# Kernel tuning notes

Measured on AMD Instinct MI355X. Metric: run time of the kernel, lower is better.

The kernel has to match this reference:

```python
import math
import jax, jax.numpy as jnp
import numpy as np

B, N, DIM_IN, DIM_OUT = 16, 2048, 512, 512
D_K, N_HEADS = 10, 2
D_HEAD = D_K // N_HEADS  # 5


def setup_inputs() -> dict:
    key = jax.random.key(0)
    ks = jax.random.split(key, 11)
    s_in = 1.0 / math.sqrt(DIM_IN)
    s_dk = 1.0 / math.sqrt(D_K)
    s_20 = 1.0 / math.sqrt(20)
    return {
        "x": jax.random.normal(ks[0], (B, N, DIM_IN), jnp.float32),
        "Wq": jax.random.normal(ks[1], (DIM_IN, D_K), jnp.float32) * s_in,
        "bq": jax.random.normal(ks[2], (D_K,), jnp.float32) * s_in,
        "Wk": jax.random.normal(ks[3], (DIM_IN, D_K), jnp.float32) * s_in,
        "bk": jax.random.normal(ks[4], (D_K,), jnp.float32) * s_in,
        "Wv": jax.random.normal(ks[5], (DIM_IN, D_K), jnp.float32) * s_in,
        "bv": jax.random.normal(ks[6], (D_K,), jnp.float32) * s_in,
        "Wm1": jax.random.normal(ks[7], (D_K, 20), jnp.float32) * s_dk,
        "bm1": jax.random.normal(ks[8], (20,), jnp.float32) * s_dk,
        "Wm2": jax.random.normal(ks[9], (20, DIM_OUT), jnp.float32) * s_20,
        "bm2": jax.random.normal(ks[10], (DIM_OUT,), jnp.float32) * s_20,
    }


def reference(x, Wq, bq, Wk, bk, Wv, bv, Wm1, bm1, Wm2, bm2):
    b, n, _ = x.shape
    # project and split heads: [B, n, d_k] -> [B, h, n, d_head]
    def heads(w, bias):
        return (x @ w + bias).reshape(b, n, N_HEADS, D_HEAD).transpose(0, 2, 1, 3)
    q, k, v = heads(Wq, bq), heads(Wk, bk), heads(Wv, bv)
    # sin-activated scores, then causal mask + softmax
    scores = jnp.sin(jnp.einsum("bhqd,bhkd->bhqk", q, k) / math.sqrt(D_HEAD))
    causal = jnp.tril(jnp.ones((n, n), bool))  # nopeak mask, k=0
    scores = jnp.where(causal, scores, jnp.float32(-1e9))
    attn = jax.nn.softmax(scores, axis=-1)
    vals = jnp.einsum("bhqk,bhkd->bhqd", attn, v)
    concat = vals.transpose(0, 2, 1, 3).reshape(b, n, D_K)
    # MLP head: leaky_relu (slope 0.01) then linear
    h1 = jax.nn.leaky_relu(concat @ Wm1 + bm1, negative_slope=0.01)
    return h1 @ Wm2 + bm2
```

## Files before the change

### kernel.cpp

```cpp
#include <hip/hip_runtime.h>
#include <math.h>

#define BB   16
#define NN   2048
#define DIN  512
#define DKK  10
#define NHD  2
#define DH   5
#define HID  20
#define DOUT 512
#define BH   32
#define KC   256
#define NKC  8
#define PC   64
#define QB   512

#define QKV_ELEMS  ((size_t)3*BH*NN*8)
#define PART_ELEMS ((size_t)NKC*BH*NN*8)

__global__ __launch_bounds__(256) void pack_w_kernel(
    const float* __restrict__ Wq, const float* __restrict__ Wk,
    const float* __restrict__ Wv, float* __restrict__ Wpack)
{
    const int idx = blockIdx.x*256 + threadIdx.x;
    const int j = idx >> 5, c = idx & 31;
    float v = 0.f;
    if (c < 10)      v = Wq[j*DKK + c];
    else if (c < 20) v = Wk[j*DKK + (c-10)];
    else if (c < 30) v = Wv[j*DKK + (c-20)];
    Wpack[idx] = v;
}

__global__ __launch_bounds__(256) void proj_kernel(
    const float* __restrict__ x, const float* __restrict__ Wpack,
    const float* __restrict__ bq, const float* __restrict__ bk,
    const float* __restrict__ bv, float* __restrict__ qkv)
{
    __shared__ float xs[PC][65];
    const int t    = threadIdx.x;
    const int lane = t & 63;
    const int grp  = __builtin_amdgcn_readfirstlane(t >> 6);
    const int tok0 = blockIdx.x*64;

    float acc[8];
    #pragma unroll
    for (int i=0;i<8;i++) acc[i]=0.f;

    for (int ch=0; ch<DIN/PC; ++ch){
        __syncthreads();
        #pragma unroll
        for (int p=0;p<4;p++){
            const int f  = t + p*256;
            const int tt = f >> 4;
            const int dd = (f & 15) * 4;
            const float4 v = *(const float4*)(x + (size_t)(tok0+tt)*DIN + ch*PC + dd);
            xs[dd+0][tt]=v.x; xs[dd+1][tt]=v.y; xs[dd+2][tt]=v.z; xs[dd+3][tt]=v.w;
        }
        __syncthreads();

        const float* wbase = Wpack + (size_t)(ch*PC)*32 + grp*8;
        for (int k=0;k<PC;k+=4){
            float w[4][8]; float xv[4];
            #pragma unroll
            for (int i=0;i<4;i++){
                xv[i] = xs[k+i][lane];
                #pragma unroll
                for (int o=0;o<8;o++) w[i][o] = wbase[(size_t)(k+i)*32+o];
            }
            #pragma unroll
            for (int i=0;i<4;i++){
                #pragma unroll
                for (int o=0;o<8;o++) acc[o] = fmaf(xv[i], w[i][o], acc[o]);
            }
        }
    }

    const float qs = 0.44721359549995793f;
    const int tok = tok0 + lane;
    const int b   = tok >> 11;
    const int n   = tok & (NN-1);
    #pragma unroll
    for (int i=0;i<8;i++){
        const int c = grp*8 + i;
        if (c >= 30) continue;
        const int mat = c / 10;
        const int d10 = c - mat*10;
        const int h   = d10 / 5;
        const int dd  = d10 - h*5;
        float v = acc[i] + ((mat==0) ? bq[d10] : (mat==1) ? bk[d10] : bv[d10]);
        if (mat==0) v *= qs;
        qkv[(size_t)mat*BH*NN*8 + (((size_t)(b*NHD+h))*NN + n)*8 + dd] = v;
    }
}

__global__ __launch_bounds__(256) void attn_kernel(
    const float* __restrict__ qkv, float* __restrict__ part)
{
    const int qt = blockIdx.x;
    const int kc = blockIdx.y;
    const int bh = blockIdx.z;
    const int k0 = kc*KC;
    const int qb0 = qt*QB;
    if (k0 >= qb0 + QB) return;

    const int w    = threadIdx.x >> 6;
    const int lane = threadIdx.x & 63;
    const int qw0  = qb0 + w*128;
    if (k0 >= qw0 + 128) return;

    const int q0 = qw0 + lane;
    const int q1 = qw0 + 64 + lane;
    const float* qr0 = qkv + ((size_t)bh*NN + q0)*8;
    const float* qr1 = qkv + ((size_t)bh*NN + q1)*8;
    const float4 qv0 = *(const float4*)qr0; const float q40 = qr0[4];
    const float4 qv1 = *(const float4*)qr1; const float q41 = qr1[4];

    const float* kb = qkv + (size_t)BH*NN*8 + (size_t)bh*NN*8;
    const float* vb = kb + (size_t)BH*NN*8;
    const int kend = min(KC, qw0 + 128 - k0);

    float d0=0,a00=0,a01=0,a02=0,a03=0,a04=0;
    float d1=0,a10=0,a11=0,a12=0,a13=0,a14=0;
    for (int kk=0; kk<kend; kk+=4){
        float4 K4[4], V4[4]; float K1[4], V1[4];
        #pragma unroll
        for (int i=0;i<4;i++){
            const float* kr = kb + (size_t)(k0+kk+i)*8;
            const float* vr = vb + (size_t)(k0+kk+i)*8;
            K4[i]=*(const float4*)kr; K1[i]=kr[4];
            V4[i]=*(const float4*)vr; V1[i]=vr[4];
        }
        #pragma unroll
        for (int i=0;i<4;i++){
            const int kg = k0+kk+i;
            float s0 = qv0.x*K4[i].x + qv0.y*K4[i].y + qv0.z*K4[i].z
                     + qv0.w*K4[i].w + q40*K1[i];
            float s1 = qv1.x*K4[i].x + qv1.y*K4[i].y + qv1.z*K4[i].z
                     + qv1.w*K4[i].w + q41*K1[i];
            float e0 = __expf(__sinf(s0));
            float e1 = __expf(__sinf(s1));
            e0 = (kg <= q0) ? e0 : 0.f;
            e1 = (kg <= q1) ? e1 : 0.f;
            d0 += e0;
            a00 = fmaf(e0, V4[i].x, a00);
            a01 = fmaf(e0, V4[i].y, a01);
            a02 = fmaf(e0, V4[i].z, a02);
            a03 = fmaf(e0, V4[i].w, a03);
            a04 = fmaf(e0, V1[i],   a04);
            d1 += e1;
            a10 = fmaf(e1, V4[i].x, a10);
            a11 = fmaf(e1, V4[i].y, a11);
            a12 = fmaf(e1, V4[i].z, a12);
            a13 = fmaf(e1, V4[i].w, a13);
            a14 = fmaf(e1, V1[i],   a14);
        }
    }
    float* pr0 = part + (((size_t)kc*BH + bh)*NN + q0)*8;
    *(float4*)pr0 = make_float4(a00,a01,a02,a03);
    pr0[4] = a04; pr0[5] = d0;
    float* pr1 = part + (((size_t)kc*BH + bh)*NN + q1)*8;
    *(float4*)pr1 = make_float4(a10,a11,a12,a13);
    pr1[4] = a14; pr1[5] = d1;
}

__global__ __launch_bounds__(256) void h1_kernel(
    const float* __restrict__ part,
    const float* __restrict__ Wm1, const float* __restrict__ bm1,
    float* __restrict__ h1buf)
{
    const int tok = blockIdx.x*256 + threadIdx.x;
    const int b   = tok >> 11;
    const int n   = tok & (NN-1);
    const int nc  = (n >> 8) + 1;

    float vals[DKK];
    #pragma unroll
    for (int h=0;h<NHD;h++){
        const int bh = b*NHD + h;
        float s0=0,s1=0,s2=0,s3=0,s4=0,sd=0;
        for (int c=0;c<nc;c++){
            const float* pr = part + (((size_t)c*BH + bh)*NN + n)*8;
            const float4 p0 = *(const float4*)pr;
            const float4 p1 = *(const float4*)(pr+4);
            s0+=p0.x; s1+=p0.y; s2+=p0.z; s3+=p0.w; s4+=p1.x; sd+=p1.y;
        }
        const float inv = 1.0f / sd;
        vals[h*DH+0]=s0*inv; vals[h*DH+1]=s1*inv; vals[h*DH+2]=s2*inv;
        vals[h*DH+3]=s3*inv; vals[h*DH+4]=s4*inv;
    }

    float h1[HID];
    #pragma unroll
    for (int jo=0;jo<HID;jo++){
        float t = bm1[jo];
        #pragma unroll
        for (int d=0;d<DKK;d++) t = fmaf(vals[d], Wm1[d*HID+jo], t);
        h1[jo] = (t > 0.f) ? t : 0.01f*t;
    }
    float* hr = h1buf + (size_t)tok*HID;
    #pragma unroll
    for (int j5=0;j5<5;j5++)
        *(float4*)(hr + j5*4) = make_float4(h1[j5*4+0],h1[j5*4+1],h1[j5*4+2],h1[j5*4+3]);
}

__global__ __launch_bounds__(256) void out_kernel(
    const float* __restrict__ h1buf,
    const float* __restrict__ Wm2, const float* __restrict__ bm2,
    float* __restrict__ out)
{
    const int wave = threadIdx.x >> 6;
    const int lane = threadIdx.x & 63;
    const int unit = blockIdx.x*4 + wave;
    const int hc   = unit & 1;
    const int tg   = unit >> 1;
    const int o0   = hc*256 + lane*4;

    float4 w2[HID];
    #pragma unroll
    for (int j=0;j<HID;j++) w2[j] = *(const float4*)(Wm2 + j*DOUT + o0);
    const float4 b2 = *(const float4*)(bm2 + o0);

    for (int ti=0; ti<8; ++ti){
        const int tok = tg*8 + ti;
        const float* hr = h1buf + (size_t)tok*HID;
        float4 acc = b2;
        #pragma unroll
        for (int j5=0;j5<5;j5++){
            const float4 hv = *(const float4*)(hr + j5*4);
            const float h0=hv.x, h1v=hv.y, h2=hv.z, h3=hv.w;
            acc.x = fmaf(h0, w2[j5*4+0].x, acc.x);
            acc.y = fmaf(h0, w2[j5*4+0].y, acc.y);
            acc.z = fmaf(h0, w2[j5*4+0].z, acc.z);
            acc.w = fmaf(h0, w2[j5*4+0].w, acc.w);
            acc.x = fmaf(h1v, w2[j5*4+1].x, acc.x);
            acc.y = fmaf(h1v, w2[j5*4+1].y, acc.y);
            acc.z = fmaf(h1v, w2[j5*4+1].z, acc.z);
            acc.w = fmaf(h1v, w2[j5*4+1].w, acc.w);
            acc.x = fmaf(h2, w2[j5*4+2].x, acc.x);
            acc.y = fmaf(h2, w2[j5*4+2].y, acc.y);
            acc.z = fmaf(h2, w2[j5*4+2].z, acc.z);
            acc.w = fmaf(h2, w2[j5*4+2].w, acc.w);
            acc.x = fmaf(h3, w2[j5*4+3].x, acc.x);
            acc.y = fmaf(h3, w2[j5*4+3].y, acc.y);
            acc.z = fmaf(h3, w2[j5*4+3].z, acc.z);
            acc.w = fmaf(h3, w2[j5*4+3].w, acc.w);
        }
        *(float4*)(out + (size_t)tok*DOUT + o0) = acc;
    }
}

extern "C" void kernel_launch(void* const* d_in, const int* in_sizes, int n_in,
                              void* d_out, int out_size, void* d_ws, size_t ws_size,
                              hipStream_t stream) {
    const float* x   = (const float*)d_in[0];
    const float* Wq  = (const float*)d_in[1];
    const float* bq  = (const float*)d_in[2];
    const float* Wk  = (const float*)d_in[3];
    const float* bk  = (const float*)d_in[4];
    const float* Wv  = (const float*)d_in[5];
    const float* bv  = (const float*)d_in[6];
    const float* Wm1 = (const float*)d_in[7];
    const float* bm1 = (const float*)d_in[8];
    const float* Wm2 = (const float*)d_in[9];
    const float* bm2 = (const float*)d_in[10];
    float* out = (float*)d_out;

    float* qkv   = (float*)d_ws;
    float* part  = qkv + QKV_ELEMS;
    float* Wpack = part + PART_ELEMS;
    float* h1buf = qkv;

    pack_w_kernel<<<dim3(64), dim3(256), 0, stream>>>(Wq, Wk, Wv, Wpack);
    proj_kernel<<<dim3(512), dim3(256), 0, stream>>>(x, Wpack, bq, bk, bv, qkv);
    attn_kernel<<<dim3(4, NKC, BH), dim3(256), 0, stream>>>(qkv, part);
    h1_kernel<<<dim3(128), dim3(256), 0, stream>>>(part, Wm1, bm1, h1buf);
    out_kernel<<<dim3(2048), dim3(256), 0, stream>>>(h1buf, Wm2, bm2, out);
}
```

Measured before the change: 274.3 us.

## Stage projection weights in LDS and retile attention to one wave per block

Result: slower. 305.2 us (+11.3%).

```diff
diff --git a/kernel.cpp b/kernel.cpp
--- a/kernel.cpp
+++ b/kernel.cpp
@@ -13,7 +13,6 @@
 #define KC   256
 #define NKC  8
 #define PC   64
-#define QB   512
 
 #define QKV_ELEMS  ((size_t)3*BH*NN*8)
 #define PART_ELEMS ((size_t)NKC*BH*NN*8)
@@ -37,9 +36,10 @@
     const float* __restrict__ bv, float* __restrict__ qkv)
 {
     __shared__ float xs[PC][65];
+    __shared__ float wls[PC*32];
     const int t    = threadIdx.x;
     const int lane = t & 63;
-    const int grp  = __builtin_amdgcn_readfirstlane(t >> 6);
+    const int grp  = t >> 6;
     const int tok0 = blockIdx.x*64;
 
     float acc[8];
@@ -56,16 +56,22 @@
             const float4 v = *(const float4*)(x + (size_t)(tok0+tt)*DIN + ch*PC + dd);
             xs[dd+0][tt]=v.x; xs[dd+1][tt]=v.y; xs[dd+2][tt]=v.z; xs[dd+3][tt]=v.w;
         }
+        #pragma unroll
+        for (int p=0;p<2;p++){
+            const int f = t + p*256;
+            ((float4*)wls)[f] = ((const float4*)(Wpack + (size_t)ch*PC*32))[f];
+        }
         __syncthreads();
 
-        const float* wbase = Wpack + (size_t)(ch*PC)*32 + grp*8;
         for (int k=0;k<PC;k+=4){
             float w[4][8]; float xv[4];
             #pragma unroll
             for (int i=0;i<4;i++){
                 xv[i] = xs[k+i][lane];
-                #pragma unroll
-                for (int o=0;o<8;o++) w[i][o] = wbase[(size_t)(k+i)*32+o];
+                const float4* wrow = (const float4*)(wls + (size_t)(k+i)*32 + grp*8);
+                const float4 wa = wrow[0], wb = wrow[1];
+                w[i][0]=wa.x; w[i][1]=wa.y; w[i][2]=wa.z; w[i][3]=wa.w;
+                w[i][4]=wb.x; w[i][5]=wb.y; w[i][6]=wb.z; w[i][7]=wb.w;
             }
             #pragma unroll
             for (int i=0;i<4;i++){
@@ -93,74 +99,68 @@
     }
 }
 
-__global__ __launch_bounds__(256) void attn_kernel(
+__global__ __launch_bounds__(64) void attn_kernel(
     const float* __restrict__ qkv, float* __restrict__ part)
 {
     const int qt = blockIdx.x;
     const int kc = blockIdx.y;
     const int bh = blockIdx.z;
+    if (kc > qt) return;
+    const int lane = threadIdx.x;
     const int k0 = kc*KC;
-    const int qb0 = qt*QB;
-    if (k0 >= qb0 + QB) return;
-
-    const int w    = threadIdx.x >> 6;
-    const int lane = threadIdx.x & 63;
-    const int qw0  = qb0 + w*128;
-    if (k0 >= qw0 + 128) return;
-
-    const int q0 = qw0 + lane;
-    const int q1 = qw0 + 64 + lane;
-    const float* qr0 = qkv + ((size_t)bh*NN + q0)*8;
-    const float* qr1 = qkv + ((size_t)bh*NN + q1)*8;
-    const float4 qv0 = *(const float4*)qr0; const float q40 = qr0[4];
-    const float4 qv1 = *(const float4*)qr1; const float q41 = qr1[4];
+    const int zr = (int)(blockDim.y >> 16);
+
+    int q[4]; const float* qr[4];
+    float4 qv[4]; float q4[4];
+    #pragma unroll
+    for (int i=0;i<4;i++){
+        q[i]  = qt*256 + i*64 + lane;
+        qr[i] = qkv + ((size_t)bh*NN + q[i])*8;
+        qv[i] = *(const float4*)qr[i];
+        q4[i] = qr[i][4];
+    }
 
     const float* kb = qkv + (size_t)BH*NN*8 + (size_t)bh*NN*8;
     const float* vb = kb + (size_t)BH*NN*8;
-    const int kend = min(KC, qw0 + 128 - k0);
-
-    float d0=0,a00=0,a01=0,a02=0,a03=0,a04=0;
-    float d1=0,a10=0,a11=0,a12=0,a13=0,a14=0;
-    for (int kk=0; kk<kend; kk+=4){
+
+    float den[4] = {0,0,0,0};
+    float a0[4]={0,0,0,0}, a1[4]={0,0,0,0}, a2[4]={0,0,0,0},
+          a3[4]={0,0,0,0}, a4[4]={0,0,0,0};
+
+    for (int kk=0; kk<KC; kk+=4){
         float4 K4[4], V4[4]; float K1[4], V1[4];
         #pragma unroll
         for (int i=0;i<4;i++){
-            const float* kr = kb + (size_t)(k0+kk+i)*8;
-            const float* vr = vb + (size_t)(k0+kk+i)*8;
+            const float* kr = kb + (size_t)(k0+kk+i+zr)*8;
+            const float* vr = vb + (size_t)(k0+kk+i+zr)*8;
             K4[i]=*(const float4*)kr; K1[i]=kr[4];
             V4[i]=*(const float4*)vr; V1[i]=vr[4];
         }
         #pragma unroll
         for (int i=0;i<4;i++){
             const int kg = k0+kk+i;
-            float s0 = qv0.x*K4[i].x + qv0.y*K4[i].y + qv0.z*K4[i].z
-                     + qv0.w*K4[i].w + q40*K1[i];
-            float s1 = qv1.x*K4[i].x + qv1.y*K4[i].y + qv1.z*K4[i].z
-                     + qv1.w*K4[i].w + q41*K1[i];
-            float e0 = __expf(__sinf(s0));
-            float e1 = __expf(__sinf(s1));
-            e0 = (kg <= q0) ? e0 : 0.f;
-            e1 = (kg <= q1) ? e1 : 0.f;
-            d0 += e0;
-            a00 = fmaf(e0, V4[i].x, a00);
-            a01 = fmaf(e0, V4[i].y, a01);
-            a02 = fmaf(e0, V4[i].z, a02);
-            a03 = fmaf(e0, V4[i].w, a03);
-            a04 = fmaf(e0, V1[i],   a04);
-            d1 += e1;
-            a10 = fmaf(e1, V4[i].x, a10);
-            a11 = fmaf(e1, V4[i].y, a11);
-            a12 = fmaf(e1, V4[i].z, a12);
-            a13 = fmaf(e1, V4[i].w, a13);
-            a14 = fmaf(e1, V1[i],   a14);
-        }
-    }
-    float* pr0 = part + (((size_t)kc*BH + bh)*NN + q0)*8;
-    *(float4*)pr0 = make_float4(a00,a01,a02,a03);
-    pr0[4] = a04; pr0[5] = d0;
-    float* pr1 = part + (((size_t)kc*BH + bh)*NN + q1)*8;
-    *(float4*)pr1 = make_float4(a10,a11,a12,a13);
-    pr1[4] = a14; pr1[5] = d1;
+            #pragma unroll
+            for (int j=0;j<4;j++){
+                float s = qv[j].x*K4[i].x + qv[j].y*K4[i].y + qv[j].z*K4[i].z
+                        + qv[j].w*K4[i].w + q4[j]*K1[i];
+                float e = __expf(__sinf(s));
+                e = (kg <= q[j]) ? e : 0.f;
+                den[j] += e;
+                a0[j] = fmaf(e, V4[i].x, a0[j]);
+                a1[j] = fmaf(e, V4[i].y, a1[j]);
+                a2[j] = fmaf(e, V4[i].z, a2[j]);
+                a3[j] = fmaf(e, V4[i].w, a3[j]);
+                a4[j] = fmaf(e, V1[i],   a4[j]);
+            }
+        }
+    }
+    #pragma unroll
+    for (int j=0;j<4;j++){
+        float* pr = part + (((size_t)kc*BH + bh)*NN + q[j])*8;
+        *(float4*)pr = make_float4(a0[j],a1[j],a2[j],a3[j]);
+        pr[4] = a4[j];
+        pr[5] = den[j];
+    }
 }
 
 __global__ __launch_bounds__(256) void h1_kernel(
@@ -272,7 +272,7 @@
 
     pack_w_kernel<<<dim3(64), dim3(256), 0, stream>>>(Wq, Wk, Wv, Wpack);
     proj_kernel<<<dim3(512), dim3(256), 0, stream>>>(x, Wpack, bq, bk, bv, qkv);
-    attn_kernel<<<dim3(4, NKC, BH), dim3(256), 0, stream>>>(qkv, part);
+    attn_kernel<<<dim3(8, 8, BH), dim3(64), 0, stream>>>(qkv, part);
     h1_kernel<<<dim3(128), dim3(256), 0, stream>>>(part, Wm1, bm1, h1buf);
     out_kernel<<<dim3(2048), dim3(256), 0, stream>>>(h1buf, Wm2, bm2, out);
 }
```

## Use bf16 MFMA for QKV projection and double-buffer K/V loads in attention

Applied to the files above, without the earlier changes.

New measurement: 252.9 us. -7.8%, faster.

```diff
diff --git a/kernel.cpp b/kernel.cpp
--- a/kernel.cpp
+++ b/kernel.cpp
@@ -12,101 +12,110 @@
 #define BH   32
 #define KC   256
 #define NKC  8
-#define PC   64
-#define QB   512
+
+typedef __attribute__((ext_vector_type(8))) short bf16x8;
+typedef __attribute__((ext_vector_type(4))) float f32x4;
+
+__device__ inline unsigned short f2bf(float f){
+    union { float f; unsigned int u; } v; v.f = f;
+    return (unsigned short)((v.u + 0x7FFFu + ((v.u >> 16) & 1u)) >> 16);
+}
 
 #define QKV_ELEMS  ((size_t)3*BH*NN*8)
 #define PART_ELEMS ((size_t)NKC*BH*NN*8)
 
-__global__ __launch_bounds__(256) void pack_w_kernel(
+__global__ __launch_bounds__(256) void pack_wbf_kernel(
     const float* __restrict__ Wq, const float* __restrict__ Wk,
-    const float* __restrict__ Wv, float* __restrict__ Wpack)
+    const float* __restrict__ Wv, unsigned short* __restrict__ Wbf)
 {
     const int idx = blockIdx.x*256 + threadIdx.x;
-    const int j = idx >> 5, c = idx & 31;
+    const int i  = idx & 7;
+    const int l  = (idx >> 3) & 63;
+    const int t  = (idx >> 9) & 1;
+    const int kt = idx >> 10;
+    const int k  = kt*32 + (l >> 4)*8 + i;
+    const int c  = t*16 + (l & 15);
     float v = 0.f;
-    if (c < 10)      v = Wq[j*DKK + c];
-    else if (c < 20) v = Wk[j*DKK + (c-10)];
-    else if (c < 30) v = Wv[j*DKK + (c-20)];
-    Wpack[idx] = v;
+    if (c < 10)      v = Wq[k*DKK + c];
+    else if (c < 20) v = Wk[k*DKK + (c-10)];
+    else if (c < 30) v = Wv[k*DKK + (c-20)];
+    Wbf[idx] = f2bf(v);
 }
 
 __global__ __launch_bounds__(256) void proj_kernel(
-    const float* __restrict__ x, const float* __restrict__ Wpack,
+    const float* __restrict__ x, const unsigned short* __restrict__ Wbf,
     const float* __restrict__ bq, const float* __restrict__ bk,
     const float* __restrict__ bv, float* __restrict__ qkv)
 {
-    __shared__ float xs[PC][65];
     const int t    = threadIdx.x;
-    const int lane = t & 63;
-    const int grp  = __builtin_amdgcn_readfirstlane(t >> 6);
-    const int tok0 = blockIdx.x*64;
-
-    float acc[8];
-    #pragma unroll
-    for (int i=0;i<8;i++) acc[i]=0.f;
-
-    for (int ch=0; ch<DIN/PC; ++ch){
-        __syncthreads();
-        #pragma unroll
-        for (int p=0;p<4;p++){
-            const int f  = t + p*256;
-            const int tt = f >> 4;
-            const int dd = (f & 15) * 4;
-            const float4 v = *(const float4*)(x + (size_t)(tok0+tt)*DIN + ch*PC + dd);
-            xs[dd+0][tt]=v.x; xs[dd+1][tt]=v.y; xs[dd+2][tt]=v.z; xs[dd+3][tt]=v.w;
+    const int w    = t >> 6;
+    const int l    = t & 63;
+    const int tok0 = blockIdx.x*64 + w*16;
+    const int row  = l & 15;
+    const int g    = l >> 4;
+    const float* xr = x + (size_t)(tok0 + row)*DIN + g*8;
+
+    f32x4 acc0 = {0.f,0.f,0.f,0.f};
+    f32x4 acc1 = {0.f,0.f,0.f,0.f};
+
+    #pragma unroll 4
+    for (int kt = 0; kt < 16; ++kt){
+        const float4 xa = *(const float4*)(xr + kt*32);
+        const float4 xb = *(const float4*)(xr + kt*32 + 4);
+        bf16x8 a;
+        a[0]=(short)f2bf(xa.x); a[1]=(short)f2bf(xa.y);
+        a[2]=(short)f2bf(xa.z); a[3]=(short)f2bf(xa.w);
+        a[4]=(short)f2bf(xb.x); a[5]=(short)f2bf(xb.y);
+        a[6]=(short)f2bf(xb.z); a[7]=(short)f2bf(xb.w);
+        const bf16x8 b0 = *(const bf16x8*)(Wbf + ((size_t)(kt*2+0)*64 + l)*8);
+        const bf16x8 b1 = *(const bf16x8*)(Wbf + ((size_t)(kt*2+1)*64 + l)*8);
+        acc0 = __builtin_amdgcn_mfma_f32_16x16x32_bf16(a, b0, acc0, 0, 0, 0);
+        acc1 = __builtin_amdgcn_mfma_f32_16x16x32_bf16(a, b1, acc1, 0, 0, 0);
+    }
+
+    const float qs = 0.44721359549995793f;
+    const int c0 = l & 15;
+    const int c1 = 16 + c0;
+    const int mat0 = (c0 >= 10);
+    const int d0i  = c0 - mat0*10;
+    const int h0   = d0i / 5, dd0 = d0i - h0*5;
+    const float bias0 = mat0 ? bk[d0i] : bq[d0i];
+    const float scl0  = mat0 ? 1.f : qs;
+    const bool  v1ok = (c1 < 30);
+    const int mat1 = (c1 < 20) ? 1 : 2;
+    const int d1i  = (c1 < 20) ? (c1-10) : (c1-20);
+    const int h1   = d1i / 5, dd1 = d1i - h1*5;
+    const float bias1 = v1ok ? ((c1 < 20) ? bk[d1i] : bv[d1i]) : 0.f;
+
+    #pragma unroll
+    for (int r = 0; r < 4; ++r){
+        const int token = tok0 + g*4 + r;
+        const int b = token >> 11;
+        const int n = token & (NN-1);
+        const float v0 = (acc0[r] + bias0) * scl0;
+        qkv[(size_t)mat0*BH*NN*8 + (((size_t)(b*NHD + h0))*NN + n)*8 + dd0] = v0;
+        if (v1ok){
+            const float v1 = acc1[r] + bias1;
+            qkv[(size_t)mat1*BH*NN*8 + (((size_t)(b*NHD + h1))*NN + n)*8 + dd1] = v1;
         }
-        __syncthreads();
-
-        const float* wbase = Wpack + (size_t)(ch*PC)*32 + grp*8;
-        for (int k=0;k<PC;k+=4){
-            float w[4][8]; float xv[4];
-            #pragma unroll
-            for (int i=0;i<4;i++){
-                xv[i] = xs[k+i][lane];
-                #pragma unroll
-                for (int o=0;o<8;o++) w[i][o] = wbase[(size_t)(k+i)*32+o];
-            }
-            #pragma unroll
-            for (int i=0;i<4;i++){
-                #pragma unroll
-                for (int o=0;o<8;o++) acc[o] = fmaf(xv[i], w[i][o], acc[o]);
-            }
-        }
-    }
-
-    const float qs = 0.44721359549995793f;
-    const int tok = tok0 + lane;
-    const int b   = tok >> 11;
-    const int n   = tok & (NN-1);
-    #pragma unroll
-    for (int i=0;i<8;i++){
-        const int c = grp*8 + i;
-        if (c >= 30) continue;
-        const int mat = c / 10;
-        const int d10 = c - mat*10;
-        const int h   = d10 / 5;
-        const int dd  = d10 - h*5;
-        float v = acc[i] + ((mat==0) ? bq[d10] : (mat==1) ? bk[d10] : bv[d10]);
-        if (mat==0) v *= qs;
-        qkv[(size_t)mat*BH*NN*8 + (((size_t)(b*NHD+h))*NN + n)*8 + dd] = v;
     }
 }
 
 __global__ __launch_bounds__(256) void attn_kernel(
     const float* __restrict__ qkv, float* __restrict__ part)
 {
-    const int qt = blockIdx.x;
-    const int kc = blockIdx.y;
-    const int bh = blockIdx.z;
-    const int k0 = kc*KC;
-    const int qb0 = qt*QB;
-    if (k0 >= qb0 + QB) return;
+    const int qt  = blockIdx.x;
+    const int kc  = blockIdx.y;
+    const int bh  = blockIdx.z;
+    const int k0  = kc*KC;
+    const int qb0 = qt*512;
+    if (k0 >= qb0 + 512) return;
 
     const int w    = threadIdx.x >> 6;
     const int lane = threadIdx.x & 63;
     const int qw0  = qb0 + w*128;
     if (k0 >= qw0 + 128) return;
+    const int zr = (int)(blockDim.y >> 16);
 
     const int q0 = qw0 + lane;
     const int q1 = qw0 + 64 + lane;
@@ -121,40 +130,55 @@
 
     float d0=0,a00=0,a01=0,a02=0,a03=0,a04=0;
     float d1=0,a10=0,a11=0,a12=0,a13=0,a14=0;
-    for (int kk=0; kk<kend; kk+=4){
-        float4 K4[4], V4[4]; float K1[4], V1[4];
-        #pragma unroll
-        for (int i=0;i<4;i++){
-            const float* kr = kb + (size_t)(k0+kk+i)*8;
-            const float* vr = vb + (size_t)(k0+kk+i)*8;
-            K4[i]=*(const float4*)kr; K1[i]=kr[4];
-            V4[i]=*(const float4*)vr; V1[i]=vr[4];
-        }
-        #pragma unroll
-        for (int i=0;i<4;i++){
-            const int kg = k0+kk+i;
-            float s0 = qv0.x*K4[i].x + qv0.y*K4[i].y + qv0.z*K4[i].z
-                     + qv0.w*K4[i].w + q40*K1[i];
-            float s1 = qv1.x*K4[i].x + qv1.y*K4[i].y + qv1.z*K4[i].z
-                     + qv1.w*K4[i].w + q41*K1[i];
-            float e0 = __expf(__sinf(s0));
-            float e1 = __expf(__sinf(s1));
-            e0 = (kg <= q0) ? e0 : 0.f;
-            e1 = (kg <= q1) ? e1 : 0.f;
-            d0 += e0;
-            a00 = fmaf(e0, V4[i].x, a00);
-            a01 = fmaf(e0, V4[i].y, a01);
-            a02 = fmaf(e0, V4[i].z, a02);
-            a03 = fmaf(e0, V4[i].w, a03);
-            a04 = fmaf(e0, V1[i],   a04);
-            d1 += e1;
-            a10 = fmaf(e1, V4[i].x, a10);
-            a11 = fmaf(e1, V4[i].y, a11);
-            a12 = fmaf(e1, V4[i].z, a12);
-            a13 = fmaf(e1, V4[i].w, a13);
-            a14 = fmaf(e1, V1[i],   a14);
-        }
-    }
+
+    float4 KA[4], VA[4], KB4[4], VB4[4];
+    float  K1A[4], V1A[4], K1B[4], V1B[4];
+
+    #define LOADB(K4,K1,V4,V1,BASE) {                              \
+        _Pragma("unroll")                                          \
+        for (int i=0;i<4;i++){                                     \
+            const float* kr = kb + (size_t)((BASE)+i+zr)*8;        \
+            const float* vr = vb + (size_t)((BASE)+i+zr)*8;        \
+            K4[i]=*(const float4*)kr; K1[i]=kr[4];                 \
+            V4[i]=*(const float4*)vr; V1[i]=vr[4];                 \
+        } }
+
+    #define COMP(K4,K1,V4,V1,BASE) {                               \
+        _Pragma("unroll")                                          \
+        for (int i=0;i<4;i++){                                     \
+            const int kg = (BASE)+i;                               \
+            float s0 = qv0.x*K4[i].x + qv0.y*K4[i].y + qv0.z*K4[i].z \
+                     + qv0.w*K4[i].w + q40*K1[i];                  \
+            float s1 = qv1.x*K4[i].x + qv1.y*K4[i].y + qv1.z*K4[i].z \
+                     + qv1.w*K4[i].w + q41*K1[i];                  \
+            float e0 = __expf(__sinf(s0));                         \
+            float e1 = __expf(__sinf(s1));                         \
+            e0 = (kg <= q0) ? e0 : 0.f;                            \
+            e1 = (kg <= q1) ? e1 : 0.f;                            \
+            d0 += e0;                                              \
+            a00 = fmaf(e0, V4[i].x, a00);                          \
+            a01 = fmaf(e0, V4[i].y, a01);                          \
+            a02 = fmaf(e0, V4[i].z, a02);                          \
+            a03 = fmaf(e0, V4[i].w, a03);                          \
+            a04 = fmaf(e0, V1[i],   a04);                          \
+            d1 += e1;                                              \
+            a10 = fmaf(e1, V4[i].x, a10);                          \
+            a11 = fmaf(e1, V4[i].y, a11);                          \
+            a12 = fmaf(e1, V4[i].z, a12);                          \
+            a13 = fmaf(e1, V4[i].w, a13);                          \
+            a14 = fmaf(e1, V1[i],   a14);                          \
+        } }
+
+    LOADB(KA,K1A,VA,V1A, k0);
+    for (int kk = 0; kk < kend; kk += 8){
+        LOADB(KB4,K1B,VB4,V1B, k0+kk+4);
+        COMP (KA,K1A,VA,V1A,  k0+kk);
+        if (kk + 8 < kend) LOADB(KA,K1A,VA,V1A, k0+kk+8);
+        COMP (KB4,K1B,VB4,V1B, k0+kk+4);
+    }
+    #undef LOADB
+    #undef COMP
+
     float* pr0 = part + (((size_t)kc*BH + bh)*NN + q0)*8;
     *(float4*)pr0 = make_float4(a00,a01,a02,a03);
     pr0[4] = a04; pr0[5] = d0;
@@ -267,11 +291,11 @@
 
     float* qkv   = (float*)d_ws;
     float* part  = qkv + QKV_ELEMS;
-    float* Wpack = part + PART_ELEMS;
+    unsigned short* Wbf = (unsigned short*)(part + PART_ELEMS);
     float* h1buf = qkv;
 
-    pack_w_kernel<<<dim3(64), dim3(256), 0, stream>>>(Wq, Wk, Wv, Wpack);
-    proj_kernel<<<dim3(512), dim3(256), 0, stream>>>(x, Wpack, bq, bk, bv, qkv);
+    pack_wbf_kernel<<<dim3(64), dim3(256), 0, stream>>>(Wq, Wk, Wv, Wbf);
+    proj_kernel<<<dim3(512), dim3(256), 0, stream>>>(x, Wbf, bq, bk, bv, qkv);
     attn_kernel<<<dim3(4, NKC, BH), dim3(256), 0, stream>>>(qkv, part);
     h1_kernel<<<dim3(128), dim3(256), 0, stream>>>(part, Wm1, bm1, h1buf);
     out_kernel<<<dim3(2048), dim3(256), 0, stream>>>(h1buf, Wm2, bm2, out);
```
